# Performance work log

Measured on AMD Instinct MI355X. Metric: run time of the kernel, lower is better.

## Reference

```python
import jax, jax.numpy as jnp
import numpy as np

V, E, H, C, T = 100000, 300, 512, 40, 4096  # vocab, embed, hidden, num_classes, seq_len


def setup_inputs() -> dict:
    key = jax.random.key(0)
    ks = jax.random.split(key, 19)
    s = lambda k, shape: jax.random.normal(k, shape, jnp.float32) * 0.05
    inp = {"x": jax.random.randint(ks[0], (T,), 0, V, dtype=jnp.int32)}
    inp["emb"] = s(ks[1], (V, E))  # frozen embedding table
    # PyTorch LSTM params, gate order (i, f, g, o); layer0 in=E, layer1 in=2H
    inp["Wih0f"] = s(ks[2], (4 * H, E)); inp["Whh0f"] = s(ks[3], (4 * H, H)); inp["b0f"] = s(ks[4], (4 * H,))
    inp["Wih0b"] = s(ks[5], (4 * H, E)); inp["Whh0b"] = s(ks[6], (4 * H, H)); inp["b0b"] = s(ks[7], (4 * H,))
    inp["Wih1f"] = s(ks[8], (4 * H, 2 * H)); inp["Whh1f"] = s(ks[9], (4 * H, H)); inp["b1f"] = s(ks[10], (4 * H,))
    inp["Wih1b"] = s(ks[11], (4 * H, 2 * H)); inp["Whh1b"] = s(ks[12], (4 * H, H)); inp["b1b"] = s(ks[13], (4 * H,))
    inp["Wc"] = s(ks[14], (C, 2 * H)); inp["bc"] = s(ks[15], (C,))
    inp["trans"] = s(ks[16], (C, C))  # CRF transitions prev->next
    inp["start"] = s(ks[17], (C,)); inp["end"] = s(ks[18], (C,))
    return inp


def _lstm_dir(x, Wih, Whh, b, reverse):
    # x: (T, D) unbatched; returns hidden states (T, H)
    Hd = Whh.shape[1]
    def step(carry, xt):
        h, c = carry
        g = xt @ Wih.T + h @ Whh.T + b  # (4H,)
        i, f, gg, o = jnp.split(g, 4)
        i = jax.nn.sigmoid(i); f = jax.nn.sigmoid(f)
        gg = jnp.tanh(gg); o = jax.nn.sigmoid(o)
        c = f * c + i * gg
        h = o * jnp.tanh(c)
        return (h, c), h
    xs = x[::-1] if reverse else x
    init = (jnp.zeros((Hd,), x.dtype), jnp.zeros((Hd,), x.dtype))
    _, hs = jax.lax.scan(step, init, xs)
    return hs[::-1] if reverse else hs


def _viterbi(emissions, trans, start, end):
    # emissions: (T, C); returns best path (T,) int32
    def fwd(score, em):
        m = score[:, None] + trans  # (C_prev, C_next)
        bp = jnp.argmax(m, axis=0).astype(jnp.int32)
        return jnp.max(m, axis=0) + em, bp
    score0 = start + emissions[0]
    final, bps = jax.lax.scan(fwd, score0, emissions[1:])  # bps: (T-1, C)
    last = jnp.argmax(final + end).astype(jnp.int32)
    def back(tag, bp):
        prev = bp[tag]
        return prev, prev
    _, path = jax.lax.scan(back, last, bps, reverse=True)  # tags 0..T-2 in order
    return jnp.concatenate([path, last[None]])


def reference(x, emb, Wih0f, Whh0f, b0f, Wih0b, Whh0b, b0b, Wih1f, Whh1f, b1f, Wih1b, Whh1b, b1b, Wc, bc, trans, start, end):
    e = emb[x]  # (T, E); dropout is identity at eval
    h0 = jnp.concatenate([_lstm_dir(e, Wih0f, Whh0f, b0f, False),
                          _lstm_dir(e, Wih0b, Whh0b, b0b, True)], axis=-1)  # (T, 2H)
    h1 = jnp.concatenate([_lstm_dir(h0, Wih1f, Whh1f, b1f, False),
                          _lstm_dir(h0, Wih1b, Whh1b, b1b, True)], axis=-1)  # (T, 2H)
    o = h1 @ Wc.T + bc  # (T, C)
    tag_scores = jax.nn.log_softmax(o, axis=1)
    tags = _viterbi(tag_scores, trans, start, end)
    return tag_scores, tags
```

## Files before the change

### kernel.cpp

```cpp
#include <hip/hip_runtime.h>


typedef unsigned int u32;
typedef unsigned long long u64;

#define TT 4096
#define HH 512
#define CC 40
#define NG 2048

__device__ __forceinline__ float sigm(float x) { return 1.0f / (1.0f + __expf(-x)); }
__device__ __forceinline__ float tanh_(float x) { return 1.0f - 2.0f / (__expf(2.0f * x) + 1.0f); }

__device__ __forceinline__ void st_agent_u32(u32* p, u32 v) {
    __hip_atomic_store(p, v, __ATOMIC_RELAXED, __HIP_MEMORY_SCOPE_AGENT);
}
__device__ __forceinline__ u64 ld_agent_u64(const u64* p) {
    return __hip_atomic_load((u64*)p, __ATOMIC_RELAXED, __HIP_MEMORY_SCOPE_AGENT);
}

__global__ __launch_bounds__(256, 2) void gemm_f32_k(const float* __restrict__ A0,
                                                     const float* __restrict__ A1,
                                                     const int* __restrict__ xidx,
                                                     const float* __restrict__ W,
                                                     const float* __restrict__ bias,
                                                     float* __restrict__ C,
                                                     int M, int N, int K, int Ksplit) {
    __shared__ float sA[32][66];
    __shared__ float sW[32][66];
    int tid = threadIdx.x;
    int bn = blockIdx.x, bm = blockIdx.y;
    int tx = tid & 15, ty = tid >> 4;
    int srow = tid >> 2, skk = (tid & 3) * 8;

    int am = bm * 64 + srow;
    const float* arow0;
    const float* arow1 = nullptr;
    if (xidx) {
        arow0 = A0 + (size_t)xidx[am] * K;
    } else {
        arow0 = A0 + (size_t)am * Ksplit;
        arow1 = A1 + (size_t)am * Ksplit;
    }
    const float* wrow = W + (size_t)(bn * 64 + srow) * K;

    float acc[4][4] = {};

    for (int kc = 0; kc < K; kc += 32) {
        float av[8], wv[8];
        if (kc + 32 <= K) {
#pragma unroll
            for (int j = 0; j < 8; j++) {
                int k = kc + skk + j;
                av[j] = (xidx || k < Ksplit) ? arow0[k] : arow1[k - Ksplit];
                wv[j] = wrow[k];
            }
        } else {
#pragma unroll
            for (int j = 0; j < 8; j++) {
                int k = kc + skk + j;
                bool ok = k < K;
                av[j] = (ok ? ((xidx || k < Ksplit) ? arow0[k] : arow1[k - Ksplit]) : 0.f);
                wv[j] = ok ? wrow[k] : 0.f;
            }
        }
        __syncthreads();
#pragma unroll
        for (int j = 0; j < 8; j++) {
            sA[skk + j][srow] = av[j];
            sW[skk + j][srow] = wv[j];
        }
        __syncthreads();
#pragma unroll
        for (int k = 0; k < 32; k++) {
            float4 a4 = *(const float4*)&sA[k][ty * 4];
            float4 w4 = *(const float4*)&sW[k][tx * 4];
            acc[0][0] += a4.x * w4.x; acc[0][1] += a4.x * w4.y; acc[0][2] += a4.x * w4.z; acc[0][3] += a4.x * w4.w;
            acc[1][0] += a4.y * w4.x; acc[1][1] += a4.y * w4.y; acc[1][2] += a4.y * w4.z; acc[1][3] += a4.y * w4.w;
            acc[2][0] += a4.z * w4.x; acc[2][1] += a4.z * w4.y; acc[2][2] += a4.z * w4.z; acc[2][3] += a4.z * w4.w;
            acc[3][0] += a4.w * w4.x; acc[3][1] += a4.w * w4.y; acc[3][2] += a4.w * w4.z; acc[3][3] += a4.w * w4.w;
        }
    }

    int gm = bm * 64 + ty * 4;
    int gn = bn * 64 + tx * 4;
    float4 b4 = *(const float4*)&bias[gn];
#pragma unroll
    for (int mi = 0; mi < 4; mi++) {
        float4 o;
        o.x = acc[mi][0] + b4.x; o.y = acc[mi][1] + b4.y;
        o.z = acc[mi][2] + b4.z; o.w = acc[mi][3] + b4.w;
        *(float4*)&C[(size_t)(gm + mi) * N + gn] = o;
    }
}

__global__ __attribute__((amdgpu_flat_work_group_size(256, 256), amdgpu_waves_per_eu(1, 1)))
void lstm_phase_k(const float* __restrict__ WxF,
                  const float* __restrict__ WxB,
                  const float* __restrict__ WhhF,
                  const float* __restrict__ WhhB,
                  float* __restrict__ histF,
                  float* __restrict__ histB,
                  int phase) {
    const int wg = blockIdx.x & 31;
    const int dir = blockIdx.x >> 5;
    const int tid = threadIdx.x;
    const float* Wx = dir ? WxB : WxF;
    const float* Whh = dir ? WhhB : WhhF;
    float* hist = dir ? histB : histF;
    const u32 ENC = phase ? 0x7F800000u : 0u;

    const int r = tid >> 2, seg = tid & 3;
    const int grow = (r >> 4) * 512 + wg * 16 + (r & 15);

    float w[128];
    {
        const float* wr = Whh + (size_t)grow * HH + seg * 128;
#pragma unroll
        for (int i = 0; i < 32; i++) {
            float4 v = *(const float4*)(wr + i * 4);
            w[i * 4 + 0] = v.x; w[i * 4 + 1] = v.y; w[i * 4 + 2] = v.z; w[i * 4 + 3] = v.w;
        }
    }

    const int j = (tid < 248) ? (tid + (tid >= wg * 8 ? 8 : 0)) : 0;

    __shared__ float lds_h[4 * 132];
    __shared__ float lds_g[64];
    float c_state = 0.f;

    for (int s = 0; s < TT; ++s) {
        const int t = dir ? (TT - 1 - s) : s;
        float wxv = 0.f;
        if (seg == 0) wxv = Wx[(size_t)t * NG + grow];

        if (s > 0) {
            const int tprev = dir ? (t + 1) : (t - 1);
            if (tid < 248) {
                const u64* p = (const u64*)(hist + (size_t)tprev * HH) + j;
                u64 v;
                int it = 0;
                for (;;) {
                    v = ld_agent_u64(p);
                    u32 lo = (u32)v, hi = (u32)(v >> 32);
                    bool ok = phase
                        ? (((lo & 0x7F800000u) >= 0x40000000u) && ((hi & 0x7F800000u) >= 0x40000000u))
                        : ((lo != 0xAAAAAAAAu) && (hi != 0xAAAAAAAAu));
                    if (ok || ++it > (1 << 20)) break;
                }
                u32 lo = (u32)v ^ ENC, hi = (u32)(v >> 32) ^ ENC;
                int idx = j * 2;
                lds_h[(idx >> 7) * 132 + (idx & 127)] = __uint_as_float(lo);
                lds_h[((idx + 1) >> 7) * 132 + ((idx + 1) & 127)] = __uint_as_float(hi);
            }
            __syncthreads();
            float acc = 0.f;
            const float4* hv4 = (const float4*)&lds_h[seg * 132];
#pragma unroll
            for (int i = 0; i < 32; i++) {
                float4 hv = hv4[i];
                acc += w[i * 4 + 0] * hv.x;
                acc += w[i * 4 + 1] * hv.y;
                acc += w[i * 4 + 2] * hv.z;
                acc += w[i * 4 + 3] * hv.w;
            }
            acc += __shfl_xor(acc, 1);
            acc += __shfl_xor(acc, 2);
            if (seg == 0) lds_g[r] = acc + wxv;
        } else {
            if (seg == 0) lds_g[r] = wxv;
        }
        __syncthreads();

        if (tid < 16) {
            float gi = lds_g[tid], gf = lds_g[16 + tid], gg = lds_g[32 + tid], go = lds_g[48 + tid];
            float iv = sigm(gi), fv = sigm(gf), gv = tanh_(gg), ov = sigm(go);
            c_state = fv * c_state + iv * gv;
            float h = ov * tanh_(c_state);
            int hidx = wg * 16 + tid;
            lds_h[(hidx >> 7) * 132 + (hidx & 127)] = h;
            st_agent_u32((u32*)&hist[(size_t)t * HH + hidx], __float_as_uint(h) ^ ENC);
        }
    }
}

__global__ __launch_bounds__(64, 4) void classifier_k(const float* __restrict__ histF,
                                                      const float* __restrict__ histB,
                                                      const float* __restrict__ Wc,
                                                      const float* __restrict__ bc,
                                                      float* __restrict__ outsc) {
    int t = blockIdx.x, lane = threadIdx.x;
    __shared__ float hrow[1024];
    const uint4* hf4 = (const uint4*)(histF + (size_t)t * HH);
    const uint4* hb4 = (const uint4*)(histB + (size_t)t * HH);
#pragma unroll
    for (int jj = 0; jj < 4; jj++) {
        int idx4 = jj * 64 + lane;
        uint4 u = (idx4 < 128) ? hf4[idx4] : hb4[idx4 - 128];
        u.x ^= 0x7F800000u; u.y ^= 0x7F800000u; u.z ^= 0x7F800000u; u.w ^= 0x7F800000u;
        float4 v;
        v.x = __uint_as_float(u.x); v.y = __uint_as_float(u.y);
        v.z = __uint_as_float(u.z); v.w = __uint_as_float(u.w);
        *(float4*)&hrow[idx4 * 4] = v;
    }
    __syncthreads();
    float o = 0.f;
    if (lane < CC) {
        o = bc[lane];
        const float4* wr = (const float4*)(Wc + (size_t)lane * 1024);
#pragma unroll 4
        for (int kk = 0; kk < 256; ++kk) {
            float4 w4 = wr[kk];
            float4 h4 = *(const float4*)&hrow[kk * 4];
            o += w4.x * h4.x + w4.y * h4.y + w4.z * h4.z + w4.w * h4.w;
        }
    }
    float m = (lane < CC) ? o : -1e30f;
#pragma unroll
    for (int d = 1; d < 64; d <<= 1) m = fmaxf(m, __shfl_xor(m, d));
    float ex = (lane < CC) ? __expf(o - m) : 0.f;
#pragma unroll
    for (int d = 1; d < 64; d <<= 1) ex += __shfl_xor(ex, d);
    float lse = m + __logf(ex);
    if (lane < CC) outsc[(size_t)t * CC + lane] = o - lse;
}

__global__ __launch_bounds__(64) void viterbi_k(const float* __restrict__ em,
                                               const float* __restrict__ trans,
                                               const float* __restrict__ startv,
                                               const float* __restrict__ endv,
                                               unsigned char* __restrict__ bp,
                                               float* __restrict__ outtags) {
    int lane = threadIdx.x;
    __shared__ float sc[64];
    float tcol[CC];
#pragma unroll
    for (int p = 0; p < CC; p++) tcol[p] = 0.f;
    if (lane < CC) {
#pragma unroll
        for (int p = 0; p < CC; p++) tcol[p] = trans[p * CC + lane];
    }
    float s = 0.f;
    if (lane < CC) s = startv[lane] + em[lane];

    for (int t = 1; t < TT; ++t) {
        if (lane < CC) sc[lane] = s;
        __syncthreads();
        float emv = (lane < CC) ? em[(size_t)t * CC + lane] : 0.f;
        float best = -1e30f;
        int bi = 0;
#pragma unroll
        for (int p = 0; p < CC; p++) {
            float cand = sc[p] + tcol[p];
            if (cand > best) { best = cand; bi = p; }
        }
        __syncthreads();
        if (lane < CC) {
            s = best + emv;
            bp[(size_t)t * CC + lane] = (unsigned char)bi;
        }
    }
    float fv = (lane < CC) ? (s + endv[lane]) : -1e30f;
    int fi = (lane < CC) ? lane : 63;
#pragma unroll
    for (int d = 1; d < 64; d <<= 1) {
        float ov = __shfl_xor(fv, d);
        int oi = __shfl_xor(fi, d);
        if (ov > fv || (ov == fv && oi < fi)) { fv = ov; fi = oi; }
    }
    __threadfence();
    __syncthreads();
    if (lane == 0) {
        int cur = fi;
        outtags[TT - 1] = (float)cur;
        for (int t = TT - 2; t >= 0; --t) {
            cur = bp[(size_t)(t + 1) * CC + cur];
            outtags[t] = (float)cur;
        }
    }
}

extern "C" void kernel_launch(void* const* d_in, const int* in_sizes, int n_in,
                              void* d_out, int out_size, void* d_ws, size_t ws_size,
                              hipStream_t stream) {
    const int*   x     = (const int*)d_in[0];
    const float* emb   = (const float*)d_in[1];
    const float* Wih0f = (const float*)d_in[2];
    const float* Whh0f = (const float*)d_in[3];
    const float* b0f   = (const float*)d_in[4];
    const float* Wih0b = (const float*)d_in[5];
    const float* Whh0b = (const float*)d_in[6];
    const float* b0b   = (const float*)d_in[7];
    const float* Wih1f = (const float*)d_in[8];
    const float* Whh1f = (const float*)d_in[9];
    const float* b1f   = (const float*)d_in[10];
    const float* Wih1b = (const float*)d_in[11];
    const float* Whh1b = (const float*)d_in[12];
    const float* b1b   = (const float*)d_in[13];
    const float* Wc    = (const float*)d_in[14];
    const float* bc    = (const float*)d_in[15];
    const float* trans = (const float*)d_in[16];
    const float* startv= (const float*)d_in[17];
    const float* endv  = (const float*)d_in[18];

    char* ws = (char*)d_ws;
    unsigned char* bp = (unsigned char*)(ws + 1024);
    float* WxF  = (float*)(ws + 262144);
    float* WxB  = (float*)(ws + 33816576);
    float* histF= (float*)(ws + 67371008);
    float* histB= (float*)(ws + 75759616);

    if (ws_size < (size_t)84148224) return;

    float* out_sc   = (float*)d_out;
    float* out_tags = out_sc + (size_t)TT * CC;

    gemm_f32_k<<<dim3(32, 64), 256, 0, stream>>>(emb, nullptr, x, Wih0f, b0f, WxF, TT, NG, 300, 300);
    gemm_f32_k<<<dim3(32, 64), 256, 0, stream>>>(emb, nullptr, x, Wih0b, b0b, WxB, TT, NG, 300, 300);
    lstm_phase_k<<<64, 256, 0, stream>>>(WxF, WxB, Whh0f, Whh0b, histF, histB, 0);
    gemm_f32_k<<<dim3(32, 64), 256, 0, stream>>>(histF, histB, nullptr, Wih1f, b1f, WxF, TT, NG, 1024, 512);
    gemm_f32_k<<<dim3(32, 64), 256, 0, stream>>>(histF, histB, nullptr, Wih1b, b1b, WxB, TT, NG, 1024, 512);
    lstm_phase_k<<<64, 256, 0, stream>>>(WxF, WxB, Whh1f, Whh1b, histF, histB, 1);
    classifier_k<<<TT, 64, 0, stream>>>(histF, histB, Wc, bc, out_sc);
    viterbi_k<<<1, 64, 0, stream>>>(out_sc, trans, startv, endv, bp, out_tags);
}
```

Baseline: 20.04 ms.

## Widen LSTM recurrence blocks to 512 threads and use shuffles in Viterbi

```diff
diff --git a/kernel.cpp b/kernel.cpp
--- a/kernel.cpp
+++ b/kernel.cpp
@@ -94,7 +94,7 @@
     }
 }
 
-__global__ __attribute__((amdgpu_flat_work_group_size(256, 256), amdgpu_waves_per_eu(1, 1)))
+__global__ __attribute__((amdgpu_flat_work_group_size(512, 512), amdgpu_waves_per_eu(2, 2)))
 void lstm_phase_k(const float* __restrict__ WxF,
                   const float* __restrict__ WxB,
                   const float* __restrict__ WhhF,
@@ -110,24 +110,25 @@
     float* hist = dir ? histB : histF;
     const u32 ENC = phase ? 0x7F800000u : 0u;
 
-    const int r = tid >> 2, seg = tid & 3;
+    const int r = tid >> 3, seg = tid & 7;
     const int grow = (r >> 4) * 512 + wg * 16 + (r & 15);
 
-    float w[128];
+    float w[64];
     {
-        const float* wr = Whh + (size_t)grow * HH + seg * 128;
-#pragma unroll
-        for (int i = 0; i < 32; i++) {
+        const float* wr = Whh + (size_t)grow * HH + seg * 64;
+#pragma unroll
+        for (int i = 0; i < 16; i++) {
             float4 v = *(const float4*)(wr + i * 4);
             w[i * 4 + 0] = v.x; w[i * 4 + 1] = v.y; w[i * 4 + 2] = v.z; w[i * 4 + 3] = v.w;
         }
     }
 
-    const int j = (tid < 248) ? (tid + (tid >= wg * 8 ? 8 : 0)) : 0;
-
-    __shared__ float lds_h[4 * 132];
+    const int j = (tid < 124) ? (tid + (tid >= wg * 4 ? 4 : 0)) : 0;
+
+    __shared__ float lds_h[8 * 68];
     __shared__ float lds_g[64];
     float c_state = 0.f;
+    int capped = 0;
 
     for (int s = 0; s < TT; ++s) {
         const int t = dir ? (TT - 1 - s) : s;
@@ -136,36 +137,49 @@
 
         if (s > 0) {
             const int tprev = dir ? (t + 1) : (t - 1);
-            if (tid < 248) {
-                const u64* p = (const u64*)(hist + (size_t)tprev * HH) + j;
-                u64 v;
-                int it = 0;
-                for (;;) {
-                    v = ld_agent_u64(p);
-                    u32 lo = (u32)v, hi = (u32)(v >> 32);
-                    bool ok = phase
-                        ? (((lo & 0x7F800000u) >= 0x40000000u) && ((hi & 0x7F800000u) >= 0x40000000u))
-                        : ((lo != 0xAAAAAAAAu) && (hi != 0xAAAAAAAAu));
-                    if (ok || ++it > (1 << 20)) break;
+            if (tid < 124) {
+                const u64* p = (const u64*)(hist + (size_t)tprev * HH) + j * 2;
+                u64 v0, v1;
+                if (!capped) {
+                    int it = 0;
+                    for (;;) {
+                        v0 = ld_agent_u64(p);
+                        v1 = ld_agent_u64(p + 1);
+                        u32 a = (u32)v0, b = (u32)(v0 >> 32), c = (u32)v1, d = (u32)(v1 >> 32);
+                        bool ok = phase
+                            ? (((a & 0x7F800000u) >= 0x40000000u) && ((b & 0x7F800000u) >= 0x40000000u) &&
+                               ((c & 0x7F800000u) >= 0x40000000u) && ((d & 0x7F800000u) >= 0x40000000u))
+                            : ((a != 0xAAAAAAAAu) && (b != 0xAAAAAAAAu) &&
+                               (c != 0xAAAAAAAAu) && (d != 0xAAAAAAAAu));
+                        if (ok) break;
+                        if (++it > (1 << 19)) { capped = 1; break; }
+                    }
+                } else {
+                    v0 = ld_agent_u64(p);
+                    v1 = ld_agent_u64(p + 1);
                 }
-                u32 lo = (u32)v ^ ENC, hi = (u32)(v >> 32) ^ ENC;
-                int idx = j * 2;
-                lds_h[(idx >> 7) * 132 + (idx & 127)] = __uint_as_float(lo);
-                lds_h[((idx + 1) >> 7) * 132 + ((idx + 1) & 127)] = __uint_as_float(hi);
+                float4 hv;
+                hv.x = __uint_as_float((u32)v0 ^ ENC);
+                hv.y = __uint_as_float((u32)(v0 >> 32) ^ ENC);
+                hv.z = __uint_as_float((u32)v1 ^ ENC);
+                hv.w = __uint_as_float((u32)(v1 >> 32) ^ ENC);
+                *(float4*)&lds_h[(j >> 4) * 68 + ((j * 4) & 63)] = hv;
             }
             __syncthreads();
-            float acc = 0.f;
-            const float4* hv4 = (const float4*)&lds_h[seg * 132];
-#pragma unroll
-            for (int i = 0; i < 32; i++) {
+            float a0 = 0.f, a1 = 0.f, a2 = 0.f, a3 = 0.f;
+            const float4* hv4 = (const float4*)&lds_h[seg * 68];
+#pragma unroll
+            for (int i = 0; i < 16; i++) {
                 float4 hv = hv4[i];
-                acc += w[i * 4 + 0] * hv.x;
-                acc += w[i * 4 + 1] * hv.y;
-                acc += w[i * 4 + 2] * hv.z;
-                acc += w[i * 4 + 3] * hv.w;
+                a0 += w[i * 4 + 0] * hv.x;
+                a1 += w[i * 4 + 1] * hv.y;
+                a2 += w[i * 4 + 2] * hv.z;
+                a3 += w[i * 4 + 3] * hv.w;
             }
+            float acc = (a0 + a1) + (a2 + a3);
             acc += __shfl_xor(acc, 1);
             acc += __shfl_xor(acc, 2);
+            acc += __shfl_xor(acc, 4);
             if (seg == 0) lds_g[r] = acc + wxv;
         } else {
             if (seg == 0) lds_g[r] = wxv;
@@ -178,7 +192,7 @@
             c_state = fv * c_state + iv * gv;
             float h = ov * tanh_(c_state);
             int hidx = wg * 16 + tid;
-            lds_h[(hidx >> 7) * 132 + (hidx & 127)] = h;
+            lds_h[(hidx >> 6) * 68 + (hidx & 63)] = h;
             st_agent_u32((u32*)&hist[(size_t)t * HH + hidx], __float_as_uint(h) ^ ENC);
         }
     }
@@ -232,7 +246,6 @@
                                                unsigned char* __restrict__ bp,
                                                float* __restrict__ outtags) {
     int lane = threadIdx.x;
-    __shared__ float sc[64];
     float tcol[CC];
 #pragma unroll
     for (int p = 0; p < CC; p++) tcol[p] = 0.f;
@@ -240,25 +253,23 @@
 #pragma unroll
         for (int p = 0; p < CC; p++) tcol[p] = trans[p * CC + lane];
     }
-    float s = 0.f;
-    if (lane < CC) s = startv[lane] + em[lane];
+    float s = (lane < CC) ? (startv[lane] + em[lane]) : 0.f;
 
     for (int t = 1; t < TT; ++t) {
-        if (lane < CC) sc[lane] = s;
-        __syncthreads();
         float emv = (lane < CC) ? em[(size_t)t * CC + lane] : 0.f;
-        float best = -1e30f;
-        int bi = 0;
-#pragma unroll
-        for (int p = 0; p < CC; p++) {
-            float cand = sc[p] + tcol[p];
-            if (cand > best) { best = cand; bi = p; }
-        }
-        __syncthreads();
-        if (lane < CC) {
-            s = best + emv;
-            bp[(size_t)t * CC + lane] = (unsigned char)bi;
-        }
+        float b0 = -1e30f, b1 = -1e30f;
+        int i0 = 0, i1 = 20;
+#pragma unroll
+        for (int p = 0; p < 20; p++) {
+            float c0 = __shfl(s, p) + tcol[p];
+            float c1 = __shfl(s, p + 20) + tcol[p + 20];
+            if (c0 > b0) { b0 = c0; i0 = p; }
+            if (c1 > b1) { b1 = c1; i1 = p + 20; }
+        }
+        float best = b0; int bi = i0;
+        if (b1 > b0) { best = b1; bi = i1; }
+        s = best + emv;
+        if (lane < CC) bp[(size_t)t * CC + lane] = (unsigned char)bi;
     }
     float fv = (lane < CC) ? (s + endv[lane]) : -1e30f;
     int fi = (lane < CC) ? lane : 63;
@@ -269,7 +280,6 @@
         if (ov > fv || (ov == fv && oi < fi)) { fv = ov; fi = oi; }
     }
     __threadfence();
-    __syncthreads();
     if (lane == 0) {
         int cur = fi;
         outtags[TT - 1] = (float)cur;
@@ -317,10 +327,10 @@
 
     gemm_f32_k<<<dim3(32, 64), 256, 0, stream>>>(emb, nullptr, x, Wih0f, b0f, WxF, TT, NG, 300, 300);
     gemm_f32_k<<<dim3(32, 64), 256, 0, stream>>>(emb, nullptr, x, Wih0b, b0b, WxB, TT, NG, 300, 300);
-    lstm_phase_k<<<64, 256, 0, stream>>>(WxF, WxB, Whh0f, Whh0b, histF, histB, 0);
+    lstm_phase_k<<<64, 512, 0, stream>>>(WxF, WxB, Whh0f, Whh0b, histF, histB, 0);
     gemm_f32_k<<<dim3(32, 64), 256, 0, stream>>>(histF, histB, nullptr, Wih1f, b1f, WxF, TT, NG, 1024, 512);
     gemm_f32_k<<<dim3(32, 64), 256, 0, stream>>>(histF, histB, nullptr, Wih1b, b1b, WxB, TT, NG, 1024, 512);
-    lstm_phase_k<<<64, 256, 0, stream>>>(WxF, WxB, Whh1f, Whh1b, histF, histB, 1);
+    lstm_phase_k<<<64, 512, 0, stream>>>(WxF, WxB, Whh1f, Whh1b, histF, histB, 1);
     classifier_k<<<TT, 64, 0, stream>>>(histF, histB, Wc, bc, out_sc);
     viterbi_k<<<1, 64, 0, stream>>>(out_sc, trans, startv, endv, bp, out_tags);
 }
```

After: 19.45 ms. 3.0% less time.
